# Optimization experiments

Measured on AMD Instinct MI355X. Metric: run time of the kernel, lower is better.

## Reference

```python
import jax, jax.numpy as jnp
import numpy as np

HEADS = 16
DIM_HEAD = 64
SCALE = DIM_HEAD ** -0.5


def setup_inputs() -> dict:
    key = jax.random.key(0)
    k1, k2, k3, k4 = jax.random.split(key, 4)
    b, n, dim = 4, 4096, 1024
    dim_inner = HEADS * DIM_HEAD
    x = jax.random.normal(k1, (b, n, dim), dtype=jnp.float32)
    W_qkv = jax.random.normal(k2, (dim, dim_inner * 3), dtype=jnp.float32) * 0.02
    agent_tokens = jax.random.normal(k3, (HEADS, 128, DIM_HEAD), dtype=jnp.float32) * 0.02
    W_out = jax.random.normal(k4, (dim_inner, dim), dtype=jnp.float32) * 0.02
    return {"x": x, "W_qkv": W_qkv, "agent_tokens": agent_tokens, "W_out": W_out}


def reference(x, W_qkv, agent_tokens, W_out):
    b, n, _ = x.shape
    h, m, d = agent_tokens.shape
    # qkv projection: b n (3 h d) -> 3, b, h, n, d
    qkv = (x @ W_qkv).reshape(b, n, 3, h, d).transpose(2, 0, 3, 1, 4)
    q, k, v = qkv[0], qkv[1], qkv[2]
    a = agent_tokens * SCALE  # h m d, broadcast over batch
    qa_sim = jnp.einsum('bhid,hjd->bhij', q, a)   # b h n m
    ak_sim = jnp.einsum('hid,bhjd->bhij', a, k)   # b h m n
    qa_attn = jax.nn.softmax(qa_sim, axis=-1)
    ak_attn = jax.nn.softmax(ak_sim, axis=-1)
    out = jnp.einsum('bhij,bhjd->bhid', ak_attn, v)    # b h m d
    out = jnp.einsum('bhij,bhjd->bhid', qa_attn, out)  # b h n d
    out = out.transpose(0, 2, 1, 3).reshape(b, n, h * d)
    return out @ W_out
```

## Files before the change

kernel.cpp:

```cpp
#include <hip/hip_runtime.h>

typedef __bf16 bf16x8 __attribute__((ext_vector_type(8)));
typedef float f32x4 __attribute__((ext_vector_type(4)));
typedef unsigned short ushort8 __attribute__((ext_vector_type(8)));
typedef unsigned short u16;

#define MFMA16(a, b, c) __builtin_amdgcn_mfma_f32_16x16x32_bf16(a, b, c, 0, 0, 0)
#define VMCNT(n) asm volatile("s_waitcnt vmcnt(" #n ")" ::: "memory")
#define SBAR() do { __builtin_amdgcn_sched_barrier(0); asm volatile("" ::: "memory"); \
                    __builtin_amdgcn_s_barrier(); \
                    asm volatile("" ::: "memory"); __builtin_amdgcn_sched_barrier(0); } while (0)

__device__ __forceinline__ u16 f2bf(float v) {
  unsigned int u = __builtin_bit_cast(unsigned int, v);
  u += 0x7fffu + ((u >> 16) & 1u);
  return (u16)(u >> 16);
}

__device__ __forceinline__ void gload16(const u16* g, u16* l) {
  __builtin_amdgcn_global_load_lds((__attribute__((address_space(1))) void*)(g),
                                   (__attribute__((address_space(3))) void*)(l), 16, 0, 0);
}


__global__ __launch_bounds__(256) void conv_x_kernel(const float* __restrict__ in, u16* __restrict__ out) {
  size_t i = (size_t)blockIdx.x * 256 + threadIdx.x;
  const float4* p = (const float4*)in + i * 2;
  float4 a = p[0], b = p[1];
  ushort8 o;
  o[0] = f2bf(a.x); o[1] = f2bf(a.y); o[2] = f2bf(a.z); o[3] = f2bf(a.w);
  o[4] = f2bf(b.x); o[5] = f2bf(b.y); o[6] = f2bf(b.z); o[7] = f2bf(b.w);
  *((ushort8*)out + i) = o;
}

__global__ __launch_bounds__(256) void conv_wT_tiled(const float* __restrict__ W, u16* __restrict__ WT,
                                                     int K, int N) {
  __shared__ float tile[64][65];
  int nt = N >> 6;
  int kt = blockIdx.x / nt, nti = blockIdx.x - kt * nt;
  int k0 = kt << 6, n0 = nti << 6;
  int t = threadIdx.x;
  int r = t >> 4, c4 = (t & 15) << 2;
#pragma unroll
  for (int j = 0; j < 4; ++j) {
    float4 v = *(const float4*)&W[(size_t)(k0 + j * 16 + r) * N + n0 + c4];
    tile[j * 16 + r][c4] = v.x; tile[j * 16 + r][c4 + 1] = v.y;
    tile[j * 16 + r][c4 + 2] = v.z; tile[j * 16 + r][c4 + 3] = v.w;
  }
  __syncthreads();
  int rn = t >> 2, cs = (t & 3) << 4;
  ushort8 o0, o1;
#pragma unroll
  for (int e = 0; e < 8; ++e) { o0[e] = f2bf(tile[cs + e][rn]); o1[e] = f2bf(tile[cs + 8 + e][rn]); }
  u16* dst = WT + (size_t)(n0 + rn) * K + k0 + cs;
  *(ushort8*)dst = o0;
  *(ushort8*)(dst + 8) = o1;
}

__global__ __launch_bounds__(256) void conv_a_kernel(const float* __restrict__ in, u16* __restrict__ out) {
  int i = blockIdx.x * 256 + threadIdx.x;
  out[i] = f2bf(in[i] * 0.125f);
}

template <int MODE>
__global__ __launch_bounds__(512, 2) void gemm256(const u16* __restrict__ A, const u16* __restrict__ BT,
                                                  int M, int N, int K,
                                                  u16* __restrict__ qb, u16* __restrict__ kb,
                                                  u16* __restrict__ vb, float* __restrict__ outf) {
  extern __shared__ char smem[];
  const int NT = K >> 5;
  int ntiles = N >> 8;
  int nwg = (M >> 8) * ntiles;
  int bid = blockIdx.x;
  int wg = (bid & 7) * (nwg >> 3) + (bid >> 3);
  int tm = wg / ntiles, tn = wg - tm * ntiles;
  int rb = tm << 8, cb = tn << 8;
  int t = threadIdx.x;
  int w = t >> 6, lane = t & 63, li = lane & 15, lg = lane >> 4;
  int wr = w >> 2, wc = w & 3;

  const u16* srcA[2];
  const u16* srcB[2];
#pragma unroll
  for (int j = 0; j < 2; ++j) {
    int D = j * 8192 + t * 16;
    int L = D ^ (((D >> 7) & 3) << 4);
    int row = L >> 6, inb = L & 63;
    srcA[j] = A + (size_t)(rb + row) * K + (inb >> 1);
    srcB[j] = BT + (size_t)(cb + row) * K + (inb >> 1);
  }
#define STAGE_A(slot, kt) do { \
    gload16(srcA[0] + (kt) * 32, (u16*)(smem + (slot) * 32768 + t * 16)); \
    gload16(srcA[1] + (kt) * 32, (u16*)(smem + (slot) * 32768 + 8192 + t * 16)); } while (0)
#define STAGE_B(slot, kt) do { \
    gload16(srcB[0] + (kt) * 32, (u16*)(smem + (slot) * 32768 + 16384 + t * 16)); \
    gload16(srcB[1] + (kt) * 32, (u16*)(smem + (slot) * 32768 + 24576 + t * 16)); } while (0)

  int offA[8], offB[4];
#pragma unroll
  for (int m8 = 0; m8 < 8; ++m8) {
    int row = wr * 128 + m8 * 16 + li;
    int L = row * 64 + lg * 16;
    offA[m8] = L ^ (((L >> 7) & 3) << 4);
  }
#pragma unroll
  for (int n = 0; n < 4; ++n) {
    int row = wc * 64 + n * 16 + li;
    int L = row * 64 + lg * 16;
    offB[n] = 16384 + (L ^ (((L >> 7) & 3) << 4));
  }

  f32x4 acc[8][4];
#pragma unroll
  for (int m = 0; m < 8; ++m)
#pragma unroll
    for (int n = 0; n < 4; ++n) acc[m][n] = (f32x4){0.f, 0.f, 0.f, 0.f};
  bf16x8 afr[4], bfr[4];

#define TILE_BODY(tt, DOSTG, WAITOP) do { \
    char* sb = smem + ((tt) & 3) * 32768; \
    afr[0] = *(const bf16x8*)(sb + offA[0]); \
    afr[1] = *(const bf16x8*)(sb + offA[1]); \
    afr[2] = *(const bf16x8*)(sb + offA[2]); \
    afr[3] = *(const bf16x8*)(sb + offA[3]); \
    bfr[0] = *(const bf16x8*)(sb + offB[0]); \
    bfr[1] = *(const bf16x8*)(sb + offB[1]); \
    bfr[2] = *(const bf16x8*)(sb + offB[2]); \
    bfr[3] = *(const bf16x8*)(sb + offB[3]); \
    if (DOSTG) STAGE_A(((tt) + 3) & 3, (tt) + 3); \
    SBAR(); \
    __builtin_amdgcn_s_setprio(1); \
    _Pragma("unroll") for (int m = 0; m < 4; ++m) \
      _Pragma("unroll") for (int n = 0; n < 4; ++n) acc[m][n] = MFMA16(afr[m], bfr[n], acc[m][n]); \
    __builtin_amdgcn_s_setprio(0); \
    SBAR(); \
    afr[0] = *(const bf16x8*)(sb + offA[4]); \
    afr[1] = *(const bf16x8*)(sb + offA[5]); \
    afr[2] = *(const bf16x8*)(sb + offA[6]); \
    afr[3] = *(const bf16x8*)(sb + offA[7]); \
    if (DOSTG) STAGE_B(((tt) + 3) & 3, (tt) + 3); \
    WAITOP; \
    SBAR(); \
    __builtin_amdgcn_s_setprio(1); \
    _Pragma("unroll") for (int m = 0; m < 4; ++m) \
      _Pragma("unroll") for (int n = 0; n < 4; ++n) acc[4 + m][n] = MFMA16(afr[m], bfr[n], acc[4 + m][n]); \
    __builtin_amdgcn_s_setprio(0); \
    SBAR(); \
  } while (0)

  STAGE_A(0, 0); STAGE_B(0, 0);
  STAGE_A(1, 1); STAGE_B(1, 1);
  STAGE_A(2, 2); STAGE_B(2, 2);
  VMCNT(8);
  SBAR();

  for (int tt = 0; tt <= NT - 4; ++tt) TILE_BODY(tt, true, VMCNT(8));
  TILE_BODY(NT - 3, false, VMCNT(4));
  TILE_BODY(NT - 2, false, VMCNT(0));
  TILE_BODY(NT - 1, false, (void)0);

  if (MODE == 0) {
    int col0 = cb + wc * 64;
    int s = col0 >> 10, hh = (col0 >> 6) & 15;
    u16* dst = (s == 0) ? qb : ((s == 1) ? kb : vb);
#pragma unroll
    for (int m = 0; m < 8; ++m) {
      int rbase = rb + wr * 128 + m * 16 + lg * 4;
#pragma unroll
      for (int r = 0; r < 4; ++r) {
        int rr = rbase + r;
        size_t o = (((size_t)(rr >> 12) * 16 + hh) * 4096 + (rr & 4095)) * 64;
#pragma unroll
        for (int n = 0; n < 4; ++n) dst[o + n * 16 + li] = f2bf(acc[m][n][r]);
      }
    }
  } else {
#pragma unroll
    for (int m = 0; m < 8; ++m) {
#pragma unroll
      for (int r = 0; r < 4; ++r) {
        float* po = outf + (size_t)(rb + wr * 128 + m * 16 + lg * 4 + r) * N + cb + wc * 64;
#pragma unroll
        for (int n = 0; n < 4; ++n) po[n * 16 + li] = acc[m][n][r];
      }
    }
  }
#undef TILE_BODY
#undef STAGE_A
#undef STAGE_B
}

__global__ __launch_bounds__(256) void transpose_v(const u16* __restrict__ v, u16* __restrict__ vt) {
  __shared__ u16 tile[64][72];
  int bid = blockIdx.x;
  int bh = bid >> 6, n0 = (bid & 63) << 6;
  int t = threadIdx.x;
  int nl = t >> 2, ds = (t & 3) << 4;
  const u16* src = v + ((size_t)bh * 4096 + n0 + nl) * 64 + ds;
  *(uint4*)&tile[nl][ds] = *(const uint4*)src;
  *(uint4*)&tile[nl][ds + 8] = *(const uint4*)(src + 8);
  __syncthreads();
  int d = t >> 2, ns = (t & 3) << 4;
  ushort8 o0, o1;
#pragma unroll
  for (int e = 0; e < 8; ++e) { o0[e] = tile[ns + e][d]; o1[e] = tile[ns + 8 + e][d]; }
  u16* dst = vt + ((size_t)bh * 64 + d) * 4096 + n0 + ns;
  *(ushort8*)dst = o0;
  *(ushort8*)(dst + 8) = o1;
}

__global__ __launch_bounds__(256) void ak_flash(const u16* __restrict__ kb, const u16* __restrict__ vt,
                                                const u16* __restrict__ ab,
                                                float* __restrict__ pO, float* __restrict__ pM,
                                                float* __restrict__ pL) {
  __shared__ u16 p_lds[128][136];
  int bid = blockIdx.x;
  int s = bid & 7;
  int bh = bid >> 3;
  int h = bh & 15;
  int t = threadIdx.x, w = t >> 6, l = t & 63, lg = l >> 4, li = l & 15;
  int jb = w * 32;

  bf16x8 afr[2][2];
#pragma unroll
  for (int jt = 0; jt < 2; ++jt)
#pragma unroll
    for (int kk = 0; kk < 2; ++kk)
      afr[jt][kk] = *(const bf16x8*)&ab[(size_t)(h * 128 + jb + jt * 16 + li) * 64 + kk * 32 + lg * 8];

  f32x4 O[2][4];
  float mrow[2][4], lrow[2][4];
#pragma unroll
  for (int jt = 0; jt < 2; ++jt) {
#pragma unroll
    for (int dt = 0; dt < 4; ++dt) O[jt][dt] = (f32x4){0.f, 0.f, 0.f, 0.f};
#pragma unroll
    for (int r = 0; r < 4; ++r) { mrow[jt][r] = -1e30f; lrow[jt][r] = 0.f; }
  }
  const u16* kbase = kb + (size_t)bh * 4096 * 64;
  const u16* vbase = vt + (size_t)bh * 64 * 4096;

  for (int c = 0; c < 4; ++c) {
    int i0 = s * 512 + c * 128;
    f32x4 sf[2][8];
#pragma unroll
    for (int jt = 0; jt < 2; ++jt)
#pragma unroll
      for (int it = 0; it < 8; ++it) sf[jt][it] = (f32x4){0.f, 0.f, 0.f, 0.f};
#pragma unroll
    for (int it = 0; it < 8; ++it)
#pragma unroll
      for (int kk = 0; kk < 2; ++kk) {
        bf16x8 bfr = *(const bf16x8*)&kbase[(size_t)(i0 + it * 16 + li) * 64 + kk * 32 + lg * 8];
        sf[0][it] = MFMA16(afr[0][kk], bfr, sf[0][it]);
        sf[1][it] = MFMA16(afr[1][kk], bfr, sf[1][it]);
      }
#pragma unroll
    for (int jt = 0; jt < 2; ++jt)
#pragma unroll
      for (int r = 0; r < 4; ++r) {
        float cm = sf[jt][0][r];
#pragma unroll
        for (int it = 1; it < 8; ++it) cm = fmaxf(cm, sf[jt][it][r]);
#pragma unroll
        for (int off = 1; off < 16; off <<= 1) cm = fmaxf(cm, __shfl_xor(cm, off));
        float mold = mrow[jt][r];
        float mnew = fmaxf(mold, cm);
        float scale = __expf(mold - mnew);
        float ss = 0.f;
#pragma unroll
        for (int it = 0; it < 8; ++it) {
          float p = __expf(sf[jt][it][r] - mnew);
          sf[jt][it][r] = p;
          ss += p;
        }
#pragma unroll
        for (int off = 1; off < 16; off <<= 1) ss += __shfl_xor(ss, off);
        lrow[jt][r] = lrow[jt][r] * scale + ss;
        mrow[jt][r] = mnew;
#pragma unroll
        for (int dt = 0; dt < 4; ++dt) O[jt][dt][r] *= scale;
      }
#pragma unroll
    for (int jt = 0; jt < 2; ++jt)
#pragma unroll
      for (int it = 0; it < 8; ++it)
#pragma unroll
        for (int r = 0; r < 4; ++r)
          p_lds[jb + jt * 16 + lg * 4 + r][it * 16 + li] = f2bf(sf[jt][it][r]);
#pragma unroll
    for (int ks = 0; ks < 4; ++ks) {
      bf16x8 pa0 = *(const bf16x8*)&p_lds[jb + li][ks * 32 + lg * 8];
      bf16x8 pa1 = *(const bf16x8*)&p_lds[jb + 16 + li][ks * 32 + lg * 8];
#pragma unroll
      for (int dt = 0; dt < 4; ++dt) {
        bf16x8 bv = *(const bf16x8*)&vbase[(size_t)(dt * 16 + li) * 4096 + i0 + ks * 32 + lg * 8];
        O[0][dt] = MFMA16(pa0, bv, O[0][dt]);
        O[1][dt] = MFMA16(pa1, bv, O[1][dt]);
      }
    }
  }
  size_t pb = ((size_t)bh * 8 + s) * 128;
#pragma unroll
  for (int jt = 0; jt < 2; ++jt)
#pragma unroll
    for (int dt = 0; dt < 4; ++dt)
#pragma unroll
      for (int r = 0; r < 4; ++r) {
        int j = jb + jt * 16 + lg * 4 + r;
        pO[(pb + j) * 64 + dt * 16 + li] = O[jt][dt][r];
      }
  if (li == 0) {
#pragma unroll
    for (int jt = 0; jt < 2; ++jt)
#pragma unroll
      for (int r = 0; r < 4; ++r) {
        int j = jb + jt * 16 + lg * 4 + r;
        pM[pb + j] = mrow[jt][r];
        pL[pb + j] = lrow[jt][r];
      }
  }
}

__global__ __launch_bounds__(128) void ak_combine(const float* __restrict__ pO, const float* __restrict__ pM,
                                                  const float* __restrict__ pL, u16* __restrict__ out1t) {
  int bh = blockIdx.x;
  int j = threadIdx.x;
  float ms[8], wv[8];
  float M = -1e30f;
#pragma unroll
  for (int s = 0; s < 8; ++s) { ms[s] = pM[((size_t)bh * 8 + s) * 128 + j]; M = fmaxf(M, ms[s]); }
  float L = 0.f;
#pragma unroll
  for (int s = 0; s < 8; ++s) { wv[s] = __expf(ms[s] - M); L += wv[s] * pL[((size_t)bh * 8 + s) * 128 + j]; }
  float inv = 1.f / L;
  for (int d = 0; d < 64; ++d) {
    float acc = 0.f;
#pragma unroll
    for (int s = 0; s < 8; ++s) acc += wv[s] * pO[(((size_t)bh * 8 + s) * 128 + j) * 64 + d];
    out1t[((size_t)bh * 64 + d) * 128 + j] = f2bf(acc * inv);
  }
}

__global__ __launch_bounds__(256) void qa_fused(const u16* __restrict__ qb, const u16* __restrict__ out1t,
                                                const u16* __restrict__ ab, u16* __restrict__ out2) {
  __shared__ u16 p_lds[128][136];
  int bid = blockIdx.x;
  int nt = bid & 31;
  int bh = bid >> 5;
  int h = bh & 15, b = bh >> 4;
  int t = threadIdx.x, w = t >> 6, l = t & 63, lg = l >> 4, li = l & 15;
  int n0 = nt * 128;

  const u16* qbase = qb + ((size_t)bh * 4096 + n0 + w * 32) * 64;
  bf16x8 qf[2][2];
#pragma unroll
  for (int rt = 0; rt < 2; ++rt)
#pragma unroll
    for (int kk = 0; kk < 2; ++kk)
      qf[rt][kk] = *(const bf16x8*)&qbase[(size_t)(rt * 16 + li) * 64 + kk * 32 + lg * 8];

  f32x4 sf[2][8];
#pragma unroll
  for (int rt = 0; rt < 2; ++rt)
#pragma unroll
    for (int jt = 0; jt < 8; ++jt) sf[rt][jt] = (f32x4){0.f, 0.f, 0.f, 0.f};

  const u16* abase = ab + h * 128 * 64;
#pragma unroll
  for (int jt = 0; jt < 8; ++jt)
#pragma unroll
    for (int kk = 0; kk < 2; ++kk) {
      bf16x8 bfr = *(const bf16x8*)&abase[(size_t)(jt * 16 + li) * 64 + kk * 32 + lg * 8];
      sf[0][jt] = MFMA16(qf[0][kk], bfr, sf[0][jt]);
      sf[1][jt] = MFMA16(qf[1][kk], bfr, sf[1][jt]);
    }
  float inv[2][4];
#pragma unroll
  for (int rt = 0; rt < 2; ++rt)
#pragma unroll
    for (int r = 0; r < 4; ++r) {
      float cm = sf[rt][0][r];
#pragma unroll
      for (int jt = 1; jt < 8; ++jt) cm = fmaxf(cm, sf[rt][jt][r]);
#pragma unroll
      for (int off = 1; off < 16; off <<= 1) cm = fmaxf(cm, __shfl_xor(cm, off));
      float ss = 0.f;
#pragma unroll
      for (int jt = 0; jt < 8; ++jt) {
        float p = __expf(sf[rt][jt][r] - cm);
        sf[rt][jt][r] = p;
        ss += p;
      }
#pragma unroll
      for (int off = 1; off < 16; off <<= 1) ss += __shfl_xor(ss, off);
      inv[rt][r] = 1.f / ss;
    }
#pragma unroll
  for (int rt = 0; rt < 2; ++rt)
#pragma unroll
    for (int jt = 0; jt < 8; ++jt)
#pragma unroll
      for (int r = 0; r < 4; ++r)
        p_lds[w * 32 + rt * 16 + lg * 4 + r][jt * 16 + li] = f2bf(sf[rt][jt][r]);

  f32x4 O[2][4];
#pragma unroll
  for (int rt = 0; rt < 2; ++rt)
#pragma unroll
    for (int dt = 0; dt < 4; ++dt) O[rt][dt] = (f32x4){0.f, 0.f, 0.f, 0.f};

  const u16* obase = out1t + (size_t)bh * 64 * 128;
#pragma unroll
  for (int ks = 0; ks < 4; ++ks) {
    bf16x8 pa0 = *(const bf16x8*)&p_lds[w * 32 + li][ks * 32 + lg * 8];
    bf16x8 pa1 = *(const bf16x8*)&p_lds[w * 32 + 16 + li][ks * 32 + lg * 8];
#pragma unroll
    for (int dt = 0; dt < 4; ++dt) {
      bf16x8 bv = *(const bf16x8*)&obase[(size_t)(dt * 16 + li) * 128 + ks * 32 + lg * 8];
      O[0][dt] = MFMA16(pa0, bv, O[0][dt]);
      O[1][dt] = MFMA16(pa1, bv, O[1][dt]);
    }
  }
#pragma unroll
  for (int rt = 0; rt < 2; ++rt)
#pragma unroll
    for (int dt = 0; dt < 4; ++dt)
#pragma unroll
      for (int r = 0; r < 4; ++r) {
        int nn = n0 + w * 32 + rt * 16 + lg * 4 + r;
        int col = h * 64 + dt * 16 + li;
        out2[((size_t)b * 4096 + nn) * 1024 + col] = f2bf(O[rt][dt][r] * inv[rt][r]);
      }
}

extern "C" void kernel_launch(void* const* d_in, const int* in_sizes, int n_in,
                              void* d_out, int out_size, void* d_ws, size_t ws_size,
                              hipStream_t stream) {
  const float* x = (const float*)d_in[0];
  const float* Wqkv = (const float*)d_in[1];
  const float* agent = (const float*)d_in[2];
  const float* Wout = (const float*)d_in[3];
  float* out = (float*)d_out;

  char* ws = (char*)d_ws;
  u16* x_bf  = (u16*)(ws + 0);
  u16* wqkvT = (u16*)(ws + 33554432);
  u16* woutT = (u16*)(ws + 39845888);
  u16* a_bf  = (u16*)(ws + 41943040);
  u16* qb    = (u16*)(ws + 42205184);
  u16* kb    = (u16*)(ws + 75759616);
  u16* vb    = (u16*)(ws + 109314048);
  u16* vt    = (u16*)(ws + 142868480);
  float* pO  = (float*)(ws + 176422912);
  float* pM  = (float*)(ws + 193200128);
  float* pL  = (float*)(ws + 193724416);
  u16* out1t = (u16*)(ws + 194248704);
  u16* out2  = x_bf;

  (void)hipFuncSetAttribute((const void*)gemm256<0>, hipFuncAttributeMaxDynamicSharedMemorySize, 131072);
  (void)hipFuncSetAttribute((const void*)gemm256<1>, hipFuncAttributeMaxDynamicSharedMemorySize, 131072);

  conv_x_kernel<<<8192, 256, 0, stream>>>(x, x_bf);
  conv_wT_tiled<<<768, 256, 0, stream>>>(Wqkv, wqkvT, 1024, 3072);
  conv_wT_tiled<<<256, 256, 0, stream>>>(Wout, woutT, 1024, 1024);
  conv_a_kernel<<<512, 256, 0, stream>>>(agent, a_bf);

  gemm256<0><<<768, 512, 131072, stream>>>(x_bf, wqkvT, 16384, 3072, 1024, qb, kb, vb, nullptr);
  transpose_v<<<4096, 256, 0, stream>>>(vb, vt);
  ak_flash<<<512, 256, 0, stream>>>(kb, vt, a_bf, pO, pM, pL);
  ak_combine<<<64, 128, 0, stream>>>(pO, pM, pL, out1t);
  qa_fused<<<2048, 256, 0, stream>>>(qb, out1t, a_bf, out2);
  gemm256<1><<<256, 512, 131072, stream>>>(out2, woutT, 16384, 1024, 1024, nullptr, nullptr, nullptr, out);
}
```

Baseline: 303.2 us.

## Software-pipeline LDS fragment reads across GEMM tiles with double-buffered B registers

Restructures the GEMM main loop so the LDS reads of A and B fragments for the next tile are issued during the current tile's second MFMA phase. The B fragments use ping-pong register buffers, and the loop is unrolled by two to swap them. This cuts the number of barriers per tile from four to two and hides LDS latency behind MFMA work. In exchange it uses more registers, which could reduce occupancy, and it changes the vmcnt wait counts, which could affect correctness if they are wrong.

```diff
diff --git a/kernel.cpp b/kernel.cpp
--- a/kernel.cpp
+++ b/kernel.cpp
@@ -115,37 +115,42 @@
   for (int m = 0; m < 8; ++m)
 #pragma unroll
     for (int n = 0; n < 4; ++n) acc[m][n] = (f32x4){0.f, 0.f, 0.f, 0.f};
-  bf16x8 afr[4], bfr[4];
-
-#define TILE_BODY(tt, DOSTG, WAITOP) do { \
-    char* sb = smem + ((tt) & 3) * 32768; \
-    afr[0] = *(const bf16x8*)(sb + offA[0]); \
-    afr[1] = *(const bf16x8*)(sb + offA[1]); \
-    afr[2] = *(const bf16x8*)(sb + offA[2]); \
-    afr[3] = *(const bf16x8*)(sb + offA[3]); \
-    bfr[0] = *(const bf16x8*)(sb + offB[0]); \
-    bfr[1] = *(const bf16x8*)(sb + offB[1]); \
-    bfr[2] = *(const bf16x8*)(sb + offB[2]); \
-    bfr[3] = *(const bf16x8*)(sb + offB[3]); \
-    if (DOSTG) STAGE_A(((tt) + 3) & 3, (tt) + 3); \
+
+  bf16x8 aF[4], aS[4], b0[4], b1[4];
+
+#define RD_A_LO(sb, d) do { d[0] = *(const bf16x8*)((sb) + offA[0]); d[1] = *(const bf16x8*)((sb) + offA[1]); \
+                            d[2] = *(const bf16x8*)((sb) + offA[2]); d[3] = *(const bf16x8*)((sb) + offA[3]); } while (0)
+#define RD_A_HI(sb, d) do { d[0] = *(const bf16x8*)((sb) + offA[4]); d[1] = *(const bf16x8*)((sb) + offA[5]); \
+                            d[2] = *(const bf16x8*)((sb) + offA[6]); d[3] = *(const bf16x8*)((sb) + offA[7]); } while (0)
+#define RD_B(sb, d)    do { d[0] = *(const bf16x8*)((sb) + offB[0]); d[1] = *(const bf16x8*)((sb) + offB[1]); \
+                            d[2] = *(const bf16x8*)((sb) + offB[2]); d[3] = *(const bf16x8*)((sb) + offB[3]); } while (0)
+
+#define PH_EVEN(t, BC, STG) do { \
     SBAR(); \
+    { char* sb_ = smem + ((t) & 3) * 32768; RD_A_HI(sb_, aS); } \
+    if (STG) STAGE_A(((t) + 3) & 3, (t) + 3); \
+    __builtin_amdgcn_sched_barrier(0); \
     __builtin_amdgcn_s_setprio(1); \
     _Pragma("unroll") for (int m = 0; m < 4; ++m) \
-      _Pragma("unroll") for (int n = 0; n < 4; ++n) acc[m][n] = MFMA16(afr[m], bfr[n], acc[m][n]); \
+      _Pragma("unroll") for (int n = 0; n < 4; ++n) acc[m][n] = MFMA16(aF[m], BC[n], acc[m][n]); \
     __builtin_amdgcn_s_setprio(0); \
-    SBAR(); \
-    afr[0] = *(const bf16x8*)(sb + offA[4]); \
-    afr[1] = *(const bf16x8*)(sb + offA[5]); \
-    afr[2] = *(const bf16x8*)(sb + offA[6]); \
-    afr[3] = *(const bf16x8*)(sb + offA[7]); \
-    if (DOSTG) STAGE_B(((tt) + 3) & 3, (tt) + 3); \
+  } while (0)
+
+#define PH_ODD(t, BC, BN, STG, RDNEXT, WAITOP) do { \
     WAITOP; \
     SBAR(); \
+    if (RDNEXT) { char* sb_ = smem + (((t) + 1) & 3) * 32768; RD_A_LO(sb_, aF); RD_B(sb_, BN); } \
+    if (STG) STAGE_B(((t) + 3) & 3, (t) + 3); \
+    __builtin_amdgcn_sched_barrier(0); \
     __builtin_amdgcn_s_setprio(1); \
     _Pragma("unroll") for (int m = 0; m < 4; ++m) \
-      _Pragma("unroll") for (int n = 0; n < 4; ++n) acc[4 + m][n] = MFMA16(afr[m], bfr[n], acc[4 + m][n]); \
+      _Pragma("unroll") for (int n = 0; n < 4; ++n) acc[4 + m][n] = MFMA16(aS[m], BC[n], acc[4 + m][n]); \
     __builtin_amdgcn_s_setprio(0); \
-    SBAR(); \
+  } while (0)
+
+#define TILE(t, BC, BN, STG, RDNEXT, WAITOP) do { \
+    PH_EVEN(t, BC, STG); \
+    PH_ODD(t, BC, BN, STG, RDNEXT, WAITOP); \
   } while (0)
 
   STAGE_A(0, 0); STAGE_B(0, 0);
@@ -153,11 +158,16 @@
   STAGE_A(2, 2); STAGE_B(2, 2);
   VMCNT(8);
   SBAR();
-
-  for (int tt = 0; tt <= NT - 4; ++tt) TILE_BODY(tt, true, VMCNT(8));
-  TILE_BODY(NT - 3, false, VMCNT(4));
-  TILE_BODY(NT - 2, false, VMCNT(0));
-  TILE_BODY(NT - 1, false, (void)0);
+  RD_A_LO(smem, aF); RD_B(smem, b0);
+
+  for (int tt = 0; tt <= NT - 6; tt += 2) {
+    TILE(tt,     b0, b1, 1, 1, VMCNT(6));
+    TILE(tt + 1, b1, b0, 1, 1, VMCNT(6));
+  }
+  TILE(NT - 4, b0, b1, 1, 1, VMCNT(6));
+  TILE(NT - 3, b1, b0, 0, 1, VMCNT(4));
+  TILE(NT - 2, b0, b1, 0, 1, VMCNT(0));
+  TILE(NT - 1, b1, b0, 0, 0, (void)0);
 
   if (MODE == 0) {
     int col0 = cb + wc * 64;
@@ -185,7 +195,12 @@
       }
     }
   }
-#undef TILE_BODY
+#undef TILE
+#undef PH_ODD
+#undef PH_EVEN
+#undef RD_A_LO
+#undef RD_A_HI
+#undef RD_B
 #undef STAGE_A
 #undef STAGE_B
 }
```

After: 299.1 us. About the same (-1.4%).
